# Optimization experiments

Measured on AMD Instinct MI355X. Metric: run time of the kernel, lower is better.

Reference implementation:

```python
import jax, jax.numpy as jnp
import numpy as np


def setup_inputs() -> dict:
    key = jax.random.key(0)
    ks = jax.random.split(key, 8)
    B, Cq, Ckv, Co, T, H, W = 2, 256, 256, 256, 8, 28, 28
    s = 1.0 / np.sqrt(Cq)
    return {
        "x": jax.random.normal(ks[0], (B, Cq, T, H, W), jnp.float32),
        "context": jax.random.normal(ks[1], (B, Ckv, T, H, W), jnp.float32),
        "wq": jax.random.normal(ks[2], (Co, Cq), jnp.float32) * s,
        "bq": jnp.zeros((Co,), jnp.float32),
        "wk": jax.random.normal(ks[3], (Co, Ckv), jnp.float32) * s,
        "bk": jnp.zeros((Co,), jnp.float32),
        "wv": jax.random.normal(ks[4], (Co, Ckv), jnp.float32) * s,
        "bv": jnp.zeros((Co,), jnp.float32),
    }


def reference(x, context, wq, bq, wk, bk, wv, bv):
    B, C, T, H, W = x.shape
    N = T * H * W
    Co = wq.shape[0]
    # 1x1x1 Conv3d == per-voxel linear projection over channels
    def proj(inp, w, b):
        y = jnp.einsum('bcthw,oc->bothw', inp, w) + b[None, :, None, None, None]
        return y.reshape(B, Co, N)  # [B, Co, N]
    q = proj(x, wq, bq).transpose(0, 2, 1)        # [B, N, Co]
    k = proj(context, wk, bk)                     # [B, Co, Nc]
    v = proj(context, wv, bv).transpose(0, 2, 1)  # [B, Nc, Co]
    scale = 1.0 / jnp.sqrt(jnp.asarray(Co, x.dtype))
    attn = jax.nn.softmax(jnp.einsum('bnc,bcm->bnm', q, k) * scale, axis=-1)
    out = jnp.einsum('bnm,bmc->bnc', attn, v)     # [B, N, Co]
    out = out.transpose(0, 2, 1).reshape(B, Co, T, H, W)
    return out + x
```

## Files before the change

### kernel.cpp

```cpp
#include <hip/hip_runtime.h>
#include <hip/hip_bf16.h>
#include <math.h>

#define BB 2
#define CC 256
#define NN 6272
#define NT16 392
#define NKB32 196
#define SCL 0.09016844005f

typedef __attribute__((ext_vector_type(8))) short s8v;
typedef __attribute__((ext_vector_type(4))) float f4v;
typedef __attribute__((ext_vector_type(4))) unsigned short us4v;

__device__ inline unsigned short f2bf(float f) {
  unsigned u = __builtin_bit_cast(unsigned, f);
  u += 0x7fffu + ((u >> 16) & 1u);
  return (unsigned short)(u >> 16);
}

__device__ inline float bf2f(unsigned short h) {
  unsigned u = (unsigned)h << 16;
  return __builtin_bit_cast(float, u);
}

__global__ __launch_bounds__(256) void wcvt_kernel(
    const float* __restrict__ wq, const float* __restrict__ wk,
    const float* __restrict__ wv, unsigned short* __restrict__ Wb)
{
  int i = (blockIdx.x * 256 + threadIdx.x) * 4;
  const float* src = (i < 65536) ? wq : (i < 131072 ? wk : wv);
  int off = i & 65535;
  float4 v = *(const float4*)(src + off);
  ushort4 o;
  o.x = f2bf(v.x); o.y = f2bf(v.y); o.z = f2bf(v.z); o.w = f2bf(v.w);
  *(ushort4*)(Wb + i) = o;
}

__global__ __launch_bounds__(256) void proj_kernel(
    const float* __restrict__ x, const float* __restrict__ ctx,
    const unsigned short* __restrict__ Wb,
    const float* __restrict__ bq, const float* __restrict__ bk,
    const float* __restrict__ bv,
    unsigned short* __restrict__ Q, unsigned short* __restrict__ Kk,
    unsigned short* __restrict__ V)
{
  const int p = blockIdx.z, b = blockIdx.y;
  const int n0 = blockIdx.x * 32;
  const int tid = threadIdx.x;
  const float* in = (p == 0 ? x : ctx) + (size_t)b * CC * NN;
  const unsigned short* W = Wb + (size_t)p * 65536;
  const float* bias = (p == 0 ? bq : (p == 1 ? bk : bv));

  __shared__ __align__(16) unsigned short lds[32][264];
  for (int it = tid; it < 2048; it += 256) {
    int c  = it >> 3;
    int n4 = (it & 7) << 2;
    float4 v = *(const float4*)(in + (size_t)c * NN + n0 + n4);
    lds[n4 + 0][c] = f2bf(v.x);
    lds[n4 + 1][c] = f2bf(v.y);
    lds[n4 + 2][c] = f2bf(v.z);
    lds[n4 + 3][c] = f2bf(v.w);
  }
  __syncthreads();

  const int lane = tid & 63, l15 = lane & 15, g = lane >> 4;
  const int obase = (tid >> 6) * 64;

  f4v acc[4][2];
#pragma unroll
  for (int mt = 0; mt < 4; ++mt) {
    float4 b4 = *(const float4*)(bias + obase + mt * 16 + g * 4);
    f4v bi = {b4.x, b4.y, b4.z, b4.w};
    acc[mt][0] = bi; acc[mt][1] = bi;
  }

#pragma unroll
  for (int ks = 0; ks < 8; ++ks) {
    s8v bf0 = *(const s8v*)(&lds[l15][ks * 32 + g * 8]);
    s8v bf1 = *(const s8v*)(&lds[16 + l15][ks * 32 + g * 8]);
#pragma unroll
    for (int mt = 0; mt < 4; ++mt) {
      s8v wa = *(const s8v*)(W + (size_t)(obase + mt * 16 + l15) * CC + ks * 32 + g * 8);
      acc[mt][0] = __builtin_amdgcn_mfma_f32_16x16x32_bf16(wa, bf0, acc[mt][0], 0, 0, 0);
      acc[mt][1] = __builtin_amdgcn_mfma_f32_16x16x32_bf16(wa, bf1, acc[mt][1], 0, 0, 0);
    }
  }

  if (p == 0) {
#pragma unroll
    for (int mt = 0; mt < 4; ++mt)
#pragma unroll
      for (int qq = 0; qq < 2; ++qq)
#pragma unroll
        for (int r = 0; r < 4; ++r)
          acc[mt][qq][r] *= SCL;
  }

  if (p < 2) {
    unsigned short* dst = (p == 0 ? Q : Kk) + (size_t)b * NN * CC;
#pragma unroll
    for (int mt = 0; mt < 4; ++mt)
#pragma unroll
      for (int qq = 0; qq < 2; ++qq) {
        ushort4 pk;
        pk.x = f2bf(acc[mt][qq][0]); pk.y = f2bf(acc[mt][qq][1]);
        pk.z = f2bf(acc[mt][qq][2]); pk.w = f2bf(acc[mt][qq][3]);
        *(ushort4*)(dst + (size_t)(n0 + qq * 16 + l15) * CC + obase + mt * 16 + g * 4) = pk;
      }
  } else {
    unsigned short* dstb = V + (size_t)b * CC * NN;
#pragma unroll
    for (int mt = 0; mt < 4; ++mt)
#pragma unroll
      for (int qq = 0; qq < 2; ++qq)
#pragma unroll
        for (int r = 0; r < 4; ++r)
          dstb[(size_t)(obase + mt * 16 + g * 4 + r) * NN + n0 + qq * 16 + l15] =
              f2bf(acc[mt][qq][r]);
  }
}

__global__ __launch_bounds__(256, 4) void attn_kernel(
    const unsigned short* __restrict__ Qg,
    const unsigned short* __restrict__ Kg,
    const unsigned short* __restrict__ Vg,
    unsigned short* __restrict__ Opart,
    float* __restrict__ ml,
    int split, int kb_base, int kb_rem)
{
  const int s     = blockIdx.x % split;
  const int stile = blockIdx.x / split;
  const int b     = stile / 98;
  const int qsup  = stile % 98;
  const int tid   = threadIdx.x;
  const int w     = tid >> 6;
  const int lane  = tid & 63;
  const int l15 = lane & 15, g = lane >> 4;
  const int qt16  = qsup * 4 + w;
  const int q0    = qt16 * 16;
  const int wid16 = b * NT16 + qt16;

  const int start = s * kb_base + (s < kb_rem ? s : kb_rem);
  const int cnt   = kb_base + (s < kb_rem ? 1 : 0);

  const unsigned short* Qb = Qg + (size_t)b * NN * CC;
  const unsigned short* Kb = Kg + (size_t)b * NN * CC;
  const unsigned short* Vb = Vg + (size_t)b * CC * NN;

  __shared__ __align__(16) unsigned short K_lds[2][32 * 256];
  __shared__ __align__(16) unsigned short V_lds[2][256 * 32];
  __shared__ __align__(16) unsigned short P_lds[4][16][36];

  s8v qf[8];
#pragma unroll
  for (int ks = 0; ks < 8; ++ks)
    qf[ks] = *(const s8v*)(Qb + (size_t)(q0 + l15) * CC + ks * 32 + g * 8);

  f4v ot[16];
  const f4v fz = {0.f, 0.f, 0.f, 0.f};
#pragma unroll
  for (int mt = 0; mt < 16; ++mt) ot[mt] = fz;

  float lsum = 0.f;

  auto stage = [&](int buf, int kb32) {
    const int kb = kb32 * 32;
#pragma unroll
    for (int i = 0; i < 8; ++i) {
      int chunk = w * 512 + i * 64 + lane;
      if (chunk < 1024) {
        int r = chunk >> 5, cc = chunk & 31;
        const unsigned short* gp =
            Kb + (size_t)(kb + r) * CC + ((cc ^ (r & 15)) << 3);
        __builtin_amdgcn_global_load_lds(
            (const __attribute__((address_space(1))) unsigned int*)gp,
            (__attribute__((address_space(3))) unsigned int*)(&K_lds[buf][chunk * 8]),
            16, 0, 0);
      } else {
        int vc = chunk - 1024;
        int ch = vc >> 2, cc = vc & 3;
        const unsigned short* gp =
            Vb + (size_t)ch * NN + kb + ((cc ^ ((ch >> 1) & 3)) << 3);
        __builtin_amdgcn_global_load_lds(
            (const __attribute__((address_space(1))) unsigned int*)gp,
            (__attribute__((address_space(3))) unsigned int*)(&V_lds[buf][vc * 8]),
            16, 0, 0);
      }
    }
  };

  stage(0, start);
  int cur = 0;

  for (int ib = 0; ib < cnt; ++ib) {
    __syncthreads();
    if (ib + 1 < cnt) stage(cur ^ 1, start + ib + 1);

    const unsigned short* Kl = &K_lds[cur][0];
    const unsigned short* Vl = &V_lds[cur][0];

    f4v st[2];
    st[0] = fz; st[1] = fz;
#pragma unroll
    for (int ks = 0; ks < 8; ++ks) {
      const int co = ((ks * 4 + g) ^ l15) << 3;
#pragma unroll
      for (int kt = 0; kt < 2; ++kt) {
        s8v ka = *(const s8v*)(Kl + (kt * 16 + l15) * 256 + co);
        st[kt] = __builtin_amdgcn_mfma_f32_16x16x32_bf16(ka, qf[ks], st[kt], 0, 0, 0);
      }
    }

#pragma unroll
    for (int kt = 0; kt < 2; ++kt) {
      float p0 = __builtin_amdgcn_exp2f(st[kt][0]);
      float p1 = __builtin_amdgcn_exp2f(st[kt][1]);
      float p2 = __builtin_amdgcn_exp2f(st[kt][2]);
      float p3 = __builtin_amdgcn_exp2f(st[kt][3]);
      lsum += (p0 + p1) + (p2 + p3);
      ushort4 pk;
      pk.x = f2bf(p0); pk.y = f2bf(p1); pk.z = f2bf(p2); pk.w = f2bf(p3);
      *(ushort4*)(&P_lds[w][l15][kt * 16 + 4 * g]) = pk;
    }

    s8v pb = *(const s8v*)(&P_lds[w][l15][g * 8]);
    const int vo = (g ^ ((l15 >> 1) & 3)) << 3;
#pragma unroll
    for (int mt = 0; mt < 16; ++mt) {
      s8v va = *(const s8v*)(Vl + (mt * 16 + l15) * 32 + vo);
      ot[mt] = __builtin_amdgcn_mfma_f32_16x16x32_bf16(va, pb, ot[mt], 0, 0, 0);
    }

    cur ^= 1;
  }

  lsum += __shfl_xor(lsum, 16);
  lsum += __shfl_xor(lsum, 32);

  unsigned short* Ob = Opart + (size_t)(wid16 * split + s) * 4096;
#pragma unroll
  for (int mt = 0; mt < 16; ++mt) {
    us4v o4;
    o4.x = f2bf(ot[mt][0]); o4.y = f2bf(ot[mt][1]);
    o4.z = f2bf(ot[mt][2]); o4.w = f2bf(ot[mt][3]);
    __builtin_nontemporal_store(o4, (us4v*)(Ob + mt * 256 + lane * 4));
  }

  if (lane < 16)
    ml[(size_t)(wid16 * split + s) * 16 + lane] = lsum;
}

__global__ __launch_bounds__(256) void merge_kernel(
    const unsigned short* __restrict__ Opart,
    const float* __restrict__ ml,
    const float* __restrict__ x,
    float* __restrict__ out,
    int split)
{
  const int wid32 = blockIdx.x;
  const int b  = wid32 / (NT16 / 2);
  const int pi = wid32 % (NT16 / 2);
  const int n0 = pi * 32;
  const int tid = threadIdx.x;
  const int w = tid >> 6;
  const int lane = tid & 63;
  const int l15 = lane & 15, g = lane >> 4;

  __shared__ float lds_o[256][33];

#pragma unroll
  for (int t = 0; t < 2; ++t) {
    const int wid16 = b * NT16 + pi * 2 + t;
    float L = 0.f;
#pragma unroll
    for (int s = 0; s < 8; ++s)
      if (s < split)
        L += ml[(size_t)(wid16 * split + s) * 16 + l15];
    const float invL = 1.f / L;

#pragma unroll
    for (int j = 0; j < 4; ++j) {
      int mt = j * 4 + w;
      float a0 = 0.f, a1 = 0.f, a2 = 0.f, a3 = 0.f;
#pragma unroll
      for (int s = 0; s < 8; ++s)
        if (s < split) {
          const us4v* Op4 = (const us4v*)(Opart + (size_t)(wid16 * split + s) * 4096);
          us4v o4 = __builtin_nontemporal_load(Op4 + mt * 64 + lane);
          a0 += bf2f(o4.x); a1 += bf2f(o4.y);
          a2 += bf2f(o4.z); a3 += bf2f(o4.w);
        }
      int c = mt * 16 + g * 4;
      int nl = t * 16 + l15;
      lds_o[c + 0][nl] = a0 * invL;
      lds_o[c + 1][nl] = a1 * invL;
      lds_o[c + 2][nl] = a2 * invL;
      lds_o[c + 3][nl] = a3 * invL;
    }
  }
  __syncthreads();

  const size_t base = (size_t)b * CC * NN + n0;
  const int n = tid & 31;
  const int c0 = tid >> 5;
#pragma unroll
  for (int cg = 0; cg < 32; ++cg) {
    int c = cg * 8 + c0;
    size_t idx = base + (size_t)c * NN + n;
    out[idx] = lds_o[c][n] + x[idx];
  }
}

extern "C" void kernel_launch(void* const* d_in, const int* in_sizes, int n_in,
                              void* d_out, int out_size, void* d_ws, size_t ws_size,
                              hipStream_t stream) {
  const float* x   = (const float*)d_in[0];
  const float* ctx = (const float*)d_in[1];
  const float* wq  = (const float*)d_in[2];
  const float* bq  = (const float*)d_in[3];
  const float* wk  = (const float*)d_in[4];
  const float* bk  = (const float*)d_in[5];
  const float* wv  = (const float*)d_in[6];
  const float* bv  = (const float*)d_in[7];
  float* out = (float*)d_out;

  const size_t sz = (size_t)BB * NN * CC;
  unsigned short* Wb = (unsigned short*)d_ws;
  unsigned short* Q  = Wb + 3 * 65536;
  unsigned short* K  = Q + sz;
  unsigned short* V  = K + sz;
  const size_t fixedB = 3 * 65536 * 2 + 3 * sz * 2;

  int split = 1;
  const int cands[3] = {5, 2, 1};
  for (int i = 0; i < 3; ++i) {
    size_t need = fixedB + (size_t)cands[i] * (BB * NT16) *
                  (4096 * sizeof(unsigned short) + 16 * sizeof(float));
    if (ws_size >= need) { split = cands[i]; break; }
  }
  unsigned short* Opart = (unsigned short*)((char*)d_ws + fixedB);
  float* ml = (float*)(Opart + (size_t)split * (BB * NT16) * 4096);
  const int kb_base = NKB32 / split, kb_rem = NKB32 % split;

  wcvt_kernel<<<dim3(192), dim3(256), 0, stream>>>(wq, wk, wv, Wb);
  proj_kernel<<<dim3(NN / 32, BB, 3), dim3(256), 0, stream>>>(
      x, ctx, Wb, bq, bk, bv, Q, K, V);
  attn_kernel<<<dim3(196 * split), dim3(256), 0, stream>>>(
      Q, K, V, Opart, ml, split, kb_base, kb_rem);
  merge_kernel<<<dim3(BB * NT16 / 2), dim3(256), 0, stream>>>(
      Opart, ml, x, out, split);
}
```

Measured before the change: 259.9 us.

## Process two 16-row query tiles per wave to reuse K/V LDS fragments

Each wave now handles 32 query rows (two 16-row tiles) instead of 16. Every K and V fragment read from LDS then feeds two MFMAs, which halves LDS traffic per FLOP and halves the number of blocks restaging the same K/V tiles. The cost is twice the accumulator registers (32 output tiles plus two Q fragment sets), so launch bounds drop to 2 blocks per CU, and there are half as many blocks to fill the GPU. The partial-output and row-sum layouts, and the merge indexing, are changed to match.

```diff
diff --git a/kernel.cpp b/kernel.cpp
--- a/kernel.cpp
+++ b/kernel.cpp
@@ -5,7 +5,7 @@
 #define BB 2
 #define CC 256
 #define NN 6272
-#define NT16 392
+#define NT32 196
 #define NKB32 196
 #define SCL 0.09016844005f
 
@@ -121,7 +121,7 @@
   }
 }
 
-__global__ __launch_bounds__(256, 4) void attn_kernel(
+__global__ __launch_bounds__(256, 2) void attn_kernel(
     const unsigned short* __restrict__ Qg,
     const unsigned short* __restrict__ Kg,
     const unsigned short* __restrict__ Vg,
@@ -131,15 +131,15 @@
 {
   const int s     = blockIdx.x % split;
   const int stile = blockIdx.x / split;
-  const int b     = stile / 98;
-  const int qsup  = stile % 98;
+  const int b     = stile / 49;
+  const int qsup  = stile % 49;
   const int tid   = threadIdx.x;
   const int w     = tid >> 6;
   const int lane  = tid & 63;
   const int l15 = lane & 15, g = lane >> 4;
-  const int qt16  = qsup * 4 + w;
-  const int q0    = qt16 * 16;
-  const int wid16 = b * NT16 + qt16;
+  const int qt32  = qsup * 4 + w;
+  const int q0    = qt32 * 32;
+  const int wid32 = b * NT32 + qt32;
 
   const int start = s * kb_base + (s < kb_rem ? s : kb_rem);
   const int cnt   = kb_base + (s < kb_rem ? 1 : 0);
@@ -150,19 +150,23 @@
 
   __shared__ __align__(16) unsigned short K_lds[2][32 * 256];
   __shared__ __align__(16) unsigned short V_lds[2][256 * 32];
-  __shared__ __align__(16) unsigned short P_lds[4][16][36];
-
-  s8v qf[8];
-#pragma unroll
-  for (int ks = 0; ks < 8; ++ks)
-    qf[ks] = *(const s8v*)(Qb + (size_t)(q0 + l15) * CC + ks * 32 + g * 8);
-
-  f4v ot[16];
+  __shared__ __align__(16) unsigned short P_lds[4][2][16][36];
+
+  s8v qf[2][8];
+#pragma unroll
+  for (int qt = 0; qt < 2; ++qt)
+#pragma unroll
+    for (int ks = 0; ks < 8; ++ks)
+      qf[qt][ks] = *(const s8v*)(Qb + (size_t)(q0 + qt * 16 + l15) * CC + ks * 32 + g * 8);
+
+  f4v ot[2][16];
   const f4v fz = {0.f, 0.f, 0.f, 0.f};
 #pragma unroll
-  for (int mt = 0; mt < 16; ++mt) ot[mt] = fz;
-
-  float lsum = 0.f;
+  for (int qt = 0; qt < 2; ++qt)
+#pragma unroll
+    for (int mt = 0; mt < 16; ++mt) ot[qt][mt] = fz;
+
+  float lsum[2] = {0.f, 0.f};
 
   auto stage = [&](int buf, int kb32) {
     const int kb = kb32 * 32;
@@ -200,55 +204,67 @@
     const unsigned short* Kl = &K_lds[cur][0];
     const unsigned short* Vl = &V_lds[cur][0];
 
-    f4v st[2];
-    st[0] = fz; st[1] = fz;
+    f4v st[2][2];
+    st[0][0] = fz; st[0][1] = fz; st[1][0] = fz; st[1][1] = fz;
 #pragma unroll
     for (int ks = 0; ks < 8; ++ks) {
       const int co = ((ks * 4 + g) ^ l15) << 3;
-#pragma unroll
-      for (int kt = 0; kt < 2; ++kt) {
-        s8v ka = *(const s8v*)(Kl + (kt * 16 + l15) * 256 + co);
-        st[kt] = __builtin_amdgcn_mfma_f32_16x16x32_bf16(ka, qf[ks], st[kt], 0, 0, 0);
+      s8v ka0 = *(const s8v*)(Kl + (l15) * 256 + co);
+      s8v ka1 = *(const s8v*)(Kl + (16 + l15) * 256 + co);
+      st[0][0] = __builtin_amdgcn_mfma_f32_16x16x32_bf16(ka0, qf[0][ks], st[0][0], 0, 0, 0);
+      st[0][1] = __builtin_amdgcn_mfma_f32_16x16x32_bf16(ka0, qf[1][ks], st[0][1], 0, 0, 0);
+      st[1][0] = __builtin_amdgcn_mfma_f32_16x16x32_bf16(ka1, qf[0][ks], st[1][0], 0, 0, 0);
+      st[1][1] = __builtin_amdgcn_mfma_f32_16x16x32_bf16(ka1, qf[1][ks], st[1][1], 0, 0, 0);
+    }
+
+#pragma unroll
+    for (int kt = 0; kt < 2; ++kt)
+#pragma unroll
+      for (int qt = 0; qt < 2; ++qt) {
+        float p0 = __builtin_amdgcn_exp2f(st[kt][qt][0]);
+        float p1 = __builtin_amdgcn_exp2f(st[kt][qt][1]);
+        float p2 = __builtin_amdgcn_exp2f(st[kt][qt][2]);
+        float p3 = __builtin_amdgcn_exp2f(st[kt][qt][3]);
+        lsum[qt] += (p0 + p1) + (p2 + p3);
+        ushort4 pk;
+        pk.x = f2bf(p0); pk.y = f2bf(p1); pk.z = f2bf(p2); pk.w = f2bf(p3);
+        *(ushort4*)(&P_lds[w][qt][l15][kt * 16 + 4 * g]) = pk;
       }
-    }
-
-#pragma unroll
-    for (int kt = 0; kt < 2; ++kt) {
-      float p0 = __builtin_amdgcn_exp2f(st[kt][0]);
-      float p1 = __builtin_amdgcn_exp2f(st[kt][1]);
-      float p2 = __builtin_amdgcn_exp2f(st[kt][2]);
-      float p3 = __builtin_amdgcn_exp2f(st[kt][3]);
-      lsum += (p0 + p1) + (p2 + p3);
-      ushort4 pk;
-      pk.x = f2bf(p0); pk.y = f2bf(p1); pk.z = f2bf(p2); pk.w = f2bf(p3);
-      *(ushort4*)(&P_lds[w][l15][kt * 16 + 4 * g]) = pk;
-    }
-
-    s8v pb = *(const s8v*)(&P_lds[w][l15][g * 8]);
+
+    s8v pb0 = *(const s8v*)(&P_lds[w][0][l15][g * 8]);
+    s8v pb1 = *(const s8v*)(&P_lds[w][1][l15][g * 8]);
     const int vo = (g ^ ((l15 >> 1) & 3)) << 3;
 #pragma unroll
     for (int mt = 0; mt < 16; ++mt) {
       s8v va = *(const s8v*)(Vl + (mt * 16 + l15) * 32 + vo);
-      ot[mt] = __builtin_amdgcn_mfma_f32_16x16x32_bf16(va, pb, ot[mt], 0, 0, 0);
+      ot[0][mt] = __builtin_amdgcn_mfma_f32_16x16x32_bf16(va, pb0, ot[0][mt], 0, 0, 0);
+      ot[1][mt] = __builtin_amdgcn_mfma_f32_16x16x32_bf16(va, pb1, ot[1][mt], 0, 0, 0);
     }
 
     cur ^= 1;
   }
 
-  lsum += __shfl_xor(lsum, 16);
-  lsum += __shfl_xor(lsum, 32);
-
-  unsigned short* Ob = Opart + (size_t)(wid16 * split + s) * 4096;
-#pragma unroll
-  for (int mt = 0; mt < 16; ++mt) {
-    us4v o4;
-    o4.x = f2bf(ot[mt][0]); o4.y = f2bf(ot[mt][1]);
-    o4.z = f2bf(ot[mt][2]); o4.w = f2bf(ot[mt][3]);
-    __builtin_nontemporal_store(o4, (us4v*)(Ob + mt * 256 + lane * 4));
-  }
-
-  if (lane < 16)
-    ml[(size_t)(wid16 * split + s) * 16 + lane] = lsum;
+#pragma unroll
+  for (int qt = 0; qt < 2; ++qt) {
+    lsum[qt] += __shfl_xor(lsum[qt], 16);
+    lsum[qt] += __shfl_xor(lsum[qt], 32);
+  }
+
+  unsigned short* Ob = Opart + (size_t)(wid32 * split + s) * 8192;
+#pragma unroll
+  for (int qt = 0; qt < 2; ++qt)
+#pragma unroll
+    for (int mt = 0; mt < 16; ++mt) {
+      us4v o4;
+      o4.x = f2bf(ot[qt][mt][0]); o4.y = f2bf(ot[qt][mt][1]);
+      o4.z = f2bf(ot[qt][mt][2]); o4.w = f2bf(ot[qt][mt][3]);
+      __builtin_nontemporal_store(o4, (us4v*)(Ob + qt * 4096 + mt * 256 + lane * 4));
+    }
+
+  if (lane < 16) {
+    ml[(size_t)(wid32 * split + s) * 32 + lane]      = lsum[0];
+    ml[(size_t)(wid32 * split + s) * 32 + 16 + lane] = lsum[1];
+  }
 }
 
 __global__ __launch_bounds__(256) void merge_kernel(
@@ -259,8 +275,8 @@
     int split)
 {
   const int wid32 = blockIdx.x;
-  const int b  = wid32 / (NT16 / 2);
-  const int pi = wid32 % (NT16 / 2);
+  const int b  = wid32 / NT32;
+  const int pi = wid32 % NT32;
   const int n0 = pi * 32;
   const int tid = threadIdx.x;
   const int w = tid >> 6;
@@ -271,12 +287,11 @@
 
 #pragma unroll
   for (int t = 0; t < 2; ++t) {
-    const int wid16 = b * NT16 + pi * 2 + t;
     float L = 0.f;
 #pragma unroll
     for (int s = 0; s < 8; ++s)
       if (s < split)
-        L += ml[(size_t)(wid16 * split + s) * 16 + l15];
+        L += ml[(size_t)(wid32 * split + s) * 32 + t * 16 + l15];
     const float invL = 1.f / L;
 
 #pragma unroll
@@ -286,7 +301,8 @@
 #pragma unroll
       for (int s = 0; s < 8; ++s)
         if (s < split) {
-          const us4v* Op4 = (const us4v*)(Opart + (size_t)(wid16 * split + s) * 4096);
+          const us4v* Op4 = (const us4v*)(Opart +
+              (size_t)(wid32 * split + s) * 8192 + t * 4096);
           us4v o4 = __builtin_nontemporal_load(Op4 + mt * 64 + lane);
           a0 += bf2f(o4.x); a1 += bf2f(o4.y);
           a2 += bf2f(o4.z); a3 += bf2f(o4.w);
@@ -335,19 +351,19 @@
   int split = 1;
   const int cands[3] = {5, 2, 1};
   for (int i = 0; i < 3; ++i) {
-    size_t need = fixedB + (size_t)cands[i] * (BB * NT16) *
-                  (4096 * sizeof(unsigned short) + 16 * sizeof(float));
+    size_t need = fixedB + (size_t)cands[i] * (BB * NT32) *
+                  (8192 * sizeof(unsigned short) + 32 * sizeof(float));
     if (ws_size >= need) { split = cands[i]; break; }
   }
   unsigned short* Opart = (unsigned short*)((char*)d_ws + fixedB);
-  float* ml = (float*)(Opart + (size_t)split * (BB * NT16) * 4096);
+  float* ml = (float*)(Opart + (size_t)split * (BB * NT32) * 8192);
   const int kb_base = NKB32 / split, kb_rem = NKB32 % split;
 
   wcvt_kernel<<<dim3(192), dim3(256), 0, stream>>>(wq, wk, wv, Wb);
   proj_kernel<<<dim3(NN / 32, BB, 3), dim3(256), 0, stream>>>(
       x, ctx, Wb, bq, bk, bv, Q, K, V);
-  attn_kernel<<<dim3(196 * split), dim3(256), 0, stream>>>(
+  attn_kernel<<<dim3(98 * split), dim3(256), 0, stream>>>(
       Q, K, V, Opart, ml, split, kb_base, kb_rem);
-  merge_kernel<<<dim3(BB * NT16 / 2), dim3(256), 0, stream>>>(
+  merge_kernel<<<dim3(BB * NT32), dim3(256), 0, stream>>>(
       Opart, ml, x, out, split);
 }
```

Result: slower. 285.7 us (+9.9%).
